# Kernel tuning notes

Hardware: AMD Instinct MI355X
Metric: run time of the kernel (lower is better)

## Reference

```python
import jax, jax.numpy as jnp
import numpy as np

B, T, HID = 1, 1024, 2048
H, DK, DV, M, KW = 16, 128, 128, 128, 4  # heads, key dim, value dim, slots, conv kernel
SCALE = DK ** -0.5
EPS = 1e-5


def short_conv(x, w):
    # causal depthwise conv1d + silu; x: [B,T,C], w: [C,K]
    K = w.shape[1]
    xp = jnp.pad(x, ((0, 0), (K - 1, 0), (0, 0)))
    t = x.shape[1]
    y = sum(xp[:, i:i + t] * w[:, i] for i in range(K))
    return jax.nn.silu(y)


def l2norm(x):
    return x * jax.lax.rsqrt(jnp.sum(x * x, axis=-1, keepdims=True) + 1e-6)


def gsa2_scan(q, k, v, w, g, beta):
    # q,k: [B,T,H,DK]  v: [B,T,H,DV]  w,g: [B,T,H,M]  beta: [B,T,H]
    b = q.shape[0]
    tm = lambda x: jnp.moveaxis(x, 1, 0)  # time-major
    Sk0 = jnp.zeros((b, H, DK, M), q.dtype)  # key->slot memory
    Sv0 = jnp.zeros((b, H, M, DV), q.dtype)  # slot->value memory

    def step(carry, xs):
        Sk, Sv = carry
        q_t, k_t, v_t, w_t, g_t, b_t = xs
        gt = jnp.exp(g_t)  # [B,H,M] gate in (0,1) since g = logsigmoid(.)
        bw = b_t[:, :, None] * w_t  # beta-scaled slot write address [B,H,M]
        Sk = Sk * gt[:, :, None, :] + k_t[..., :, None] * bw[:, :, None, :]
        Sv = Sv * gt[..., None] + bw[..., None] * v_t[:, :, None, :]
        s = jnp.einsum('bhd,bhdm->bhm', q_t, Sk) * SCALE
        a = jax.nn.softmax(s, axis=-1)
        o_t = jnp.einsum('bhm,bhmd->bhd', a, Sv)
        return (Sk, Sv), o_t

    (_, _), o = jax.lax.scan(step, (Sk0, Sv0),
                             (tm(q), tm(k), tm(v), tm(w), tm(g), tm(beta)))
    return jnp.moveaxis(o, 0, 1)  # [B,T,H,DV]


def reference(hidden_states, Wq, Wk, Wv, Ww, cq, ck, cv,
              Wf1, Wf2, Wb, Wg1, Wg2, bg2, norm_w, Wo):
    h = hidden_states  # [B,T,HID]
    q = short_conv(h @ Wq, cq)
    k = short_conv(h @ Wk, ck)
    v = short_conv(h @ Wv, cv)
    w = short_conv(h @ Ww, cv)  # source applies v_conv1d to w (faithful)
    g = jax.nn.log_sigmoid((h @ Wf1) @ Wf2)   # [B,T,H*M]
    beta = jax.nn.sigmoid(h @ Wb)             # [B,T,H]
    rs = lambda x, d: x.reshape(x.shape[0], x.shape[1], -1, d)
    q, k = rs(q, DK), rs(k, DK)
    v = rs(v, DV)
    w = l2norm(rs(w, M))
    g = rs(g, M)
    o = gsa2_scan(q, k, v, w, g, beta)        # [B,T,H,DV]
    gate = rs((h @ Wg1) @ Wg2 + bg2, DV)
    # FusedRMSNormGated with sigmoid activation
    o = o * jax.lax.rsqrt(jnp.mean(o * o, axis=-1, keepdims=True) + EPS)
    o = o * norm_w * jax.nn.sigmoid(gate)
    o = o.reshape(o.shape[0], o.shape[1], -1)
    return o @ Wo


def setup_inputs() -> dict:
    key = jax.random.key(0)
    ks = jax.random.split(key, 16)
    s = 0.02
    return {
        'hidden_states': jax.random.normal(ks[0], (B, T, HID), jnp.float32),
        'Wq': jax.random.normal(ks[1], (HID, H * DK), jnp.float32) * s,
        'Wk': jax.random.normal(ks[2], (HID, H * DK), jnp.float32) * s,
        'Wv': jax.random.normal(ks[3], (HID, H * DV), jnp.float32) * s,
        'Ww': jax.random.normal(ks[4], (HID, H * M), jnp.float32) * s,
        'cq': jax.random.normal(ks[5], (H * DK, KW), jnp.float32) * 0.2,
        'ck': jax.random.normal(ks[6], (H * DK, KW), jnp.float32) * 0.2,
        'cv': jax.random.normal(ks[7], (H * DV, KW), jnp.float32) * 0.2,
        'Wf1': jax.random.normal(ks[8], (HID, DV), jnp.float32) * s,
        'Wf2': jax.random.normal(ks[9], (DV, H * M), jnp.float32) * s,
        'Wb': jax.random.normal(ks[10], (HID, H), jnp.float32) * s,
        'Wg1': jax.random.normal(ks[11], (HID, DV), jnp.float32) * s,
        'Wg2': jax.random.normal(ks[12], (DV, H * DV), jnp.float32) * s,
        'bg2': jnp.zeros((H * DV,), jnp.float32),
        'norm_w': jnp.ones((DV,), jnp.float32),
        'Wo': jax.random.normal(ks[13], (H * DV, HID), jnp.float32) * s,
    }
```

## Files before the change

### kernel.cpp

```cpp
#include <hip/hip_runtime.h>
#include <hip/hip_bf16.h>
#include <stdint.h>

typedef unsigned short u16;
typedef __attribute__((ext_vector_type(8))) short bf16x8;
typedef __attribute__((ext_vector_type(4))) short bf16x4;
typedef __attribute__((ext_vector_type(4))) float f32x4;

#define DEV static __device__ __forceinline__

DEV u16 f2bf(float f){
  union { float f; unsigned u; } x; x.f = f;
  unsigned r = x.u + 0x7fffu + ((x.u >> 16) & 1u);
  return (u16)(r >> 16);
}

DEV float bf2f(u16 u){
  union { unsigned u; float f; } x; x.u = ((unsigned)u) << 16; return x.f;
}

DEV bf16x8 ldfrag(const u16* p){
  bf16x4 a = *(const bf16x4*)p;
  bf16x4 b = *(const bf16x4*)(p+4);
  bf16x8 r;
  r[0]=a[0]; r[1]=a[1]; r[2]=a[2]; r[3]=a[3];
  r[4]=b[0]; r[5]=b[1]; r[6]=b[2]; r[7]=b[3];
  return r;
}

DEV bf16x4 cvt4(float a, float b, float c, float d){
  bf16x4 r; r[0]=(short)f2bf(a); r[1]=(short)f2bf(b); r[2]=(short)f2bf(c); r[3]=(short)f2bf(d);
  return r;
}

DEV void g2l16(const void* g, void* l){
  __builtin_amdgcn_global_load_lds((const __attribute__((address_space(1))) unsigned int*)g,
                                   (__attribute__((address_space(3))) unsigned int*)l,
                                   16, 0, 0);
}

__global__ __launch_bounds__(256)
void transp64_k(const float* __restrict__ Wq, const float* __restrict__ Wk,
                const float* __restrict__ Wv, const float* __restrict__ Ww,
                const float* __restrict__ Wo, u16* __restrict__ WcatT, u16* __restrict__ WoT,
                const float* __restrict__ hX, u16* __restrict__ h_bf,
                const float* __restrict__ Wf1, const float* __restrict__ Wg1,
                const float* __restrict__ Wf2, const float* __restrict__ Wg2,
                const float* __restrict__ Wb,
                u16* __restrict__ WfgT, u16* __restrict__ Wf2T, u16* __restrict__ Wg2T){
  __shared__ float tile[64*65];
  const int z = blockIdx.z;
  if (z == 5){
    int idx = ((blockIdx.y*32 + blockIdx.x)*256 + threadIdx.x)*8;
    float4 v0 = *(const float4*)&hX[idx];
    float4 v1 = *(const float4*)&hX[idx+4];
    ushort4 o0, o1;
    o0.x=f2bf(v0.x); o0.y=f2bf(v0.y); o0.z=f2bf(v0.z); o0.w=f2bf(v0.w);
    o1.x=f2bf(v1.x); o1.y=f2bf(v1.y); o1.z=f2bf(v1.z); o1.w=f2bf(v1.w);
    *(ushort4*)&h_bf[idx]   = o0;
    *(ushort4*)&h_bf[idx+4] = o1;
    return;
  }
  if (z == 10){
    int rem = blockIdx.y*32 + blockIdx.x;
    if (rem >= 256) return;
    int cx = rem & 63, cy = rem >> 6;
    const int x = threadIdx.x & 31, y0 = threadIdx.x >> 5;
    int k = cx*32 + x;
#pragma unroll
    for (int j=0;j<4;j++){
      int rpad = cy*32 + y0 + j*8;
      float v = (rpad < 16) ? Wb[(size_t)k*16 + rpad] : 0.f;
      WfgT[(size_t)(256+rpad)*2048 + k] = f2bf(v);
    }
    return;
  }
  if (z >= 6){
    int rem = blockIdx.y*32 + blockIdx.x;
    if (rem >= 256) return;
    const float* src; u16* dst; int R, C, cx, cy;
    if (z==6){      src=Wf1; dst=WfgT;                  R=2048; C=128;  cx=rem&3;  cy=rem>>2; }
    else if (z==7){ src=Wg1; dst=WfgT+(size_t)128*2048; R=2048; C=128;  cx=rem&3;  cy=rem>>2; }
    else if (z==8){ src=Wf2; dst=Wf2T;                  R=128;  C=2048; cx=rem>>2; cy=rem&3; }
    else {          src=Wg2; dst=Wg2T;                  R=128;  C=2048; cx=rem>>2; cy=rem&3; }
    const int c0 = cx*32, r0 = cy*32;
    const int x = threadIdx.x & 31, y0 = threadIdx.x >> 5;
#pragma unroll
    for (int j=0;j<4;j++){
      int r = y0 + j*8;
      tile[r*33 + x] = src[(size_t)(r0+r)*C + c0 + x];
    }
    __syncthreads();
#pragma unroll
    for (int j=0;j<4;j++){
      int cc = y0 + j*8;
      dst[(size_t)(c0+cc)*R + r0 + x] = f2bf(tile[x*33 + cc]);
    }
    return;
  }
  const float* src = (z==0)?Wq:((z==1)?Wk:((z==2)?Wv:((z==3)?Ww:Wo)));
  u16* dst = (z<4) ? (WcatT + (size_t)z*4194304) : WoT;
  const int c0 = blockIdx.x*64, r0 = blockIdx.y*64;
#pragma unroll
  for (int p=0;p<4;p++){
    int i = threadIdx.x + p*256;
    int r = i>>4, c4 = (i&15)<<2;
    *(float4*)&tile[r*65 + c4] = *(const float4*)&src[(size_t)(r0+r)*2048 + c0 + c4];
  }
  __syncthreads();
#pragma unroll
  for (int p=0;p<4;p++){
    int i = threadIdx.x + p*256;
    int cc = i>>4, r4 = (i&15)<<2;
    ushort4 o;
    o.x = f2bf(tile[(r4+0)*65 + cc]); o.y = f2bf(tile[(r4+1)*65 + cc]);
    o.z = f2bf(tile[(r4+2)*65 + cc]); o.w = f2bf(tile[(r4+3)*65 + cc]);
    *(ushort4*)&dst[(size_t)(c0+cc)*2048 + r0 + r4] = o;
  }
}

template<bool OBF>
__global__ __launch_bounds__(256)
void gemm4_k(const u16* __restrict__ A, const u16* __restrict__ B, void* __restrict__ Cp,
             int K, int lda, int ldb, int ldc){
  __shared__ u16 As[2][128*64];
  __shared__ u16 Bs[2][128*64];
  const int m0 = blockIdx.y*128, n0 = blockIdx.x*128;
  const int tid = threadIdx.x;
  const int wave = tid>>6, lane = tid&63, lr = lane&15, kg = lane>>4;
  const int wm = wave>>1, wn = wave&1;
  const f32x4 vz = {0.f,0.f,0.f,0.f};
  f32x4 acc[4][4];
#pragma unroll
  for (int a=0;a<4;a++)
#pragma unroll
    for (int b=0;b<4;b++) acc[a][b]=vz;

#define STAGE4(buf, k0) do { \
    _Pragma("unroll") \
    for (int p=0;p<4;p++){ \
      int chunk = tid + p*256, r_ = chunk>>3, ci = chunk&7; \
      g2l16(A + (size_t)(m0+r_)*lda + (k0) + ((ci^(r_&7))<<3), &As[buf][chunk*8]); \
    } \
    _Pragma("unroll") \
    for (int p=0;p<4;p++){ \
      int chunk = tid + p*256, r_ = chunk>>3, ci = chunk&7; \
      g2l16(B + (size_t)(n0+r_)*ldb + (k0) + ((ci^(r_&7))<<3), &Bs[buf][chunk*8]); \
    } \
  } while(0)

  const int nt = K>>6;
  STAGE4(0, 0);
  STAGE4(1, 64);
  for (int t=0; t<nt; ++t){
    const int buf = t&1;
    if (t < nt-1) asm volatile("s_waitcnt vmcnt(8)" ::: "memory");
    else          asm volatile("s_waitcnt vmcnt(0)" ::: "memory");
    asm volatile("s_barrier" ::: "memory");
#pragma unroll
    for (int ks=0; ks<2; ++ks){
      bf16x8 af[4], bfv[4];
#pragma unroll
      for (int mi=0;mi<4;mi++){
        int r = wm*64+mi*16+lr;
        af[mi] = *(const bf16x8*)&As[buf][r*64 + (((ks*4+kg)^(r&7))<<3)];
      }
#pragma unroll
      for (int ni=0;ni<4;ni++){
        int r = wn*64+ni*16+lr;
        bfv[ni] = *(const bf16x8*)&Bs[buf][r*64 + (((ks*4+kg)^(r&7))<<3)];
      }
      asm volatile("s_waitcnt lgkmcnt(0)" ::: "memory");
      __builtin_amdgcn_sched_barrier(0);
      __builtin_amdgcn_s_setprio(1);
#pragma unroll
      for (int mi=0;mi<4;mi++)
#pragma unroll
        for (int ni=0;ni<4;ni++)
          acc[mi][ni] = __builtin_amdgcn_mfma_f32_16x16x32_bf16(af[mi], bfv[ni], acc[mi][ni], 0, 0, 0);
      __builtin_amdgcn_s_setprio(0);
      __builtin_amdgcn_sched_barrier(0);
      asm volatile("s_barrier" ::: "memory");
    }
    if (t+2 < nt) STAGE4(buf, (t+2)<<6);
  }
#undef STAGE4
#pragma unroll
  for (int mi=0;mi<4;mi++)
#pragma unroll
    for (int ni=0;ni<4;ni++)
#pragma unroll
      for (int vv=0;vv<4;vv++){
        int row = m0 + wm*64 + mi*16 + kg*4 + vv;
        int col = n0 + wn*64 + ni*16 + lr;
        if (OBF) ((u16*)Cp)[(size_t)row*ldc + col] = f2bf(acc[mi][ni][vv]);
        else     ((float*)Cp)[(size_t)row*ldc + col] = acc[mi][ni][vv];
      }
}

__global__ __launch_bounds__(256)
void gemm4sk_k(const u16* __restrict__ A, const u16* __restrict__ B, float* __restrict__ out,
               int Khalf, int lda, int ldb, int ldc){
  __shared__ u16 As[2][128*64];
  __shared__ u16 Bs[2][128*64];
  const int m0 = blockIdx.y*128, n0 = blockIdx.x*128;
  const int kbase = blockIdx.z*Khalf;
  const int tid = threadIdx.x;
  const int wave = tid>>6, lane = tid&63, lr = lane&15, kg = lane>>4;
  const int wm = wave>>1, wn = wave&1;
  const f32x4 vz = {0.f,0.f,0.f,0.f};
  f32x4 acc[4][4];
#pragma unroll
  for (int a=0;a<4;a++)
#pragma unroll
    for (int b=0;b<4;b++) acc[a][b]=vz;

#define STAGE4(buf, k0) do { \
    _Pragma("unroll") \
    for (int p=0;p<4;p++){ \
      int chunk = tid + p*256, r_ = chunk>>3, ci = chunk&7; \
      g2l16(A + (size_t)(m0+r_)*lda + (k0) + ((ci^(r_&7))<<3), &As[buf][chunk*8]); \
    } \
    _Pragma("unroll") \
    for (int p=0;p<4;p++){ \
      int chunk = tid + p*256, r_ = chunk>>3, ci = chunk&7; \
      g2l16(B + (size_t)(n0+r_)*ldb + (k0) + ((ci^(r_&7))<<3), &Bs[buf][chunk*8]); \
    } \
  } while(0)

  const int nt = Khalf>>6;
  STAGE4(0, kbase);
  STAGE4(1, kbase+64);
  for (int t=0; t<nt; ++t){
    const int buf = t&1;
    if (t < nt-1) asm volatile("s_waitcnt vmcnt(8)" ::: "memory");
    else          asm volatile("s_waitcnt vmcnt(0)" ::: "memory");
    asm volatile("s_barrier" ::: "memory");
#pragma unroll
    for (int ks=0; ks<2; ++ks){
      bf16x8 af[4], bfv[4];
#pragma unroll
      for (int mi=0;mi<4;mi++){
        int r = wm*64+mi*16+lr;
        af[mi] = *(const bf16x8*)&As[buf][r*64 + (((ks*4+kg)^(r&7))<<3)];
      }
#pragma unroll
      for (int ni=0;ni<4;ni++){
        int r = wn*64+ni*16+lr;
        bfv[ni] = *(const bf16x8*)&Bs[buf][r*64 + (((ks*4+kg)^(r&7))<<3)];
// ... 66 lines not shown
  if (zz == 0){
#pragma unroll
    for (int ni=0;ni<4;ni++){
      float p[4][4]; float s[4];
#pragma unroll
      for (int mi=0;mi<4;mi++){
        float run = 0.f;
#pragma unroll
        for (int vv=0;vv<4;vv++){
          float v = acc[mi][ni][vv];
          v = fminf(v,0.f) - __logf(1.f + __expf(-fabsf(v)));
          run += v; p[mi][vv] = run;
        }
        s[mi] = run;
      }
      float M = 0.f; float base[4];
#pragma unroll
      for (int mi=0;mi<4;mi++){
        float a0 = __shfl(s[mi], lr);
        float a1 = __shfl(s[mi], lr+16);
        float a2 = __shfl(s[mi], lr+32);
        float a3 = __shfl(s[mi], lr+48);
        float before = 0.f;
        if (kg>0) before += a0;
        if (kg>1) before += a1;
        if (kg>2) before += a2;
        base[mi] = M + before;
        M += a0+a1+a2+a3;
      }
#pragma unroll
      for (int mi=0;mi<4;mi++)
#pragma unroll
        for (int vv=0;vv<4;vv++){
          int row = m0 + wr*64 + mi*16 + kg*4 + vv;
          int col = n0 + wc*64 + ni*16 + lr;
          Ccg[(size_t)row*2048 + col] = base[mi] + p[mi][vv];
        }
    }
  } else {
#pragma unroll
    for (int mi=0;mi<4;mi++)
#pragma unroll
      for (int ni=0;ni<4;ni++)
#pragma unroll
        for (int vv=0;vv<4;vv++){
          int row = m0 + wr*64 + mi*16 + kg*4 + vv;
          int col = n0 + wc*64 + ni*16 + lr;
          Cgate[(size_t)row*2048 + col] = f2bf(acc[mi][ni][vv]);
        }
  }
}

__global__ __launch_bounds__(256)
void gemmsk_k(const u16* __restrict__ A, const u16* __restrict__ B, u16* __restrict__ P,
              int lda, int ldb){
  __shared__ u16 As[128*32];
  __shared__ u16 Bs[128*32];
  const int m0 = blockIdx.y*128, n0 = blockIdx.x*128;
  const int kbase = blockIdx.z*128;
  const int tid = threadIdx.x;
  const int lane = tid & 63, wave = tid >> 6;
  const int wr = wave >> 1, wc = wave & 1;
  const int lr = lane & 15, kg = lane >> 4;
  const f32x4 vzero = {0.f,0.f,0.f,0.f};
  f32x4 acc[4][4];
#pragma unroll
  for (int a=0;a<4;a++)
#pragma unroll
    for (int b=0;b<4;b++) acc[a][b] = vzero;
  const int r0 = tid>>2, s0 = tid&3;
  for (int k0=kbase;k0<kbase+128;k0+=32){
    __syncthreads();
    g2l16(A + (size_t)(m0+r0)*lda + k0 + s0*8, (u16*)As + (size_t)tid*8);
    g2l16(B + (size_t)(n0+r0)*ldb + k0 + s0*8, (u16*)Bs + (size_t)tid*8);
    g2l16(A + (size_t)(m0+r0+64)*lda + k0 + s0*8, (u16*)As + (size_t)(tid+256)*8);
    g2l16(B + (size_t)(n0+r0+64)*ldb + k0 + s0*8, (u16*)Bs + (size_t)(tid+256)*8);
    __syncthreads();
    bf16x8 af[4], bfv[4];
#pragma unroll
    for (int mi=0;mi<4;mi++) af[mi]  = *(const bf16x8*)(As + (wr*64+mi*16+lr)*32 + kg*8);
#pragma unroll
    for (int ni=0;ni<4;ni++) bfv[ni] = *(const bf16x8*)(Bs + (wc*64+ni*16+lr)*32 + kg*8);
#pragma unroll
    for (int mi=0;mi<4;mi++)
#pragma unroll
      for (int ni=0;ni<4;ni++)
        acc[mi][ni] = __builtin_amdgcn_mfma_f32_16x16x32_bf16(af[mi], bfv[ni], acc[mi][ni], 0, 0, 0);
  }
#pragma unroll
  for (int mi=0;mi<4;mi++)
#pragma unroll
    for (int ni=0;ni<4;ni++)
#pragma unroll
      for (int vv=0;vv<4;vv++){
        int row = m0 + wr*64 + mi*16 + kg*4 + vv;
        int col = n0 + wc*64 + ni*16 + lr;
        P[(size_t)blockIdx.z*393216 + (size_t)row*384 + col] = f2bf(acc[mi][ni][vv]);
      }
}

__global__ __launch_bounds__(256)
void reduceb_k(const u16* __restrict__ P, u16* __restrict__ out, float* __restrict__ betab){
  int i4 = (blockIdx.x*256 + threadIdx.x)*4;
  float s0=0.f, s1=0.f, s2=0.f, s3=0.f;
#pragma unroll
  for (int z=0;z<16;z++){
    ushort4 p = *(const ushort4*)&P[(size_t)z*393216 + i4];
    s0+=bf2f(p.x); s1+=bf2f(p.y); s2+=bf2f(p.z); s3+=bf2f(p.w);
  }
  ushort4 o; o.x=f2bf(s0); o.y=f2bf(s1); o.z=f2bf(s2); o.w=f2bf(s3);
  *(ushort4*)&out[i4] = o;
  int col = i4 % 384;
  if (col >= 256 && col < 272){
    int row = i4 / 384;
    float* bp = &betab[row*16 + (col-256)];
    bp[0] = 1.f/(1.f+__expf(-s0));
    bp[1] = 1.f/(1.f+__expf(-s1));
    bp[2] = 1.f/(1.f+__expf(-s2));
    bp[3] = 1.f/(1.f+__expf(-s3));
  }
}

__global__ __launch_bounds__(256)
void conv_k(const u16* __restrict__ raw, const float* __restrict__ cq,
            const float* __restrict__ ck, const float* __restrict__ cv,
            const float* __restrict__ betab,
            u16* __restrict__ qo, u16* __restrict__ ko,
            u16* __restrict__ vo, u16* __restrict__ bwout){
  __shared__ float red[2][2][4];
  int idx = blockIdx.x*256 + threadIdx.x;
  int cgl = idx & 8191, tb = idx >> 13;
  int which = cgl >> 11, cc = cgl & 2047;
  const float* wt = (which==0)?cq:((which==1)?ck:cv);
  float4 w4 = *(const float4*)&wt[cc*4];
  int t0 = tb*4;
  float x[7];
#pragma unroll
  for (int j=0;j<7;j++){
    int t = t0 - 3 + j;
    x[j] = (t >= 0) ? bf2f(raw[(size_t)t*8192 + cgl]) : 0.f;
  }
  float y[4];
#pragma unroll
  for (int j=0;j<4;j++){
    float yy = x[j]*w4.x + x[j+1]*w4.y + x[j+2]*w4.z + x[j+3]*w4.w;
    y[j] = yy / (1.f + __expf(-yy));
  }
  if (which < 3){
    u16* outb = (which==0)?qo:((which==1)?ko:vo);
#pragma unroll
    for (int j=0;j<4;j++)
      outb[(size_t)(t0+j)*2048 + cc] = f2bf(y[j]);
  } else {
    const int hh = threadIdx.x >> 7;
    const int wh = (threadIdx.x >> 6) & 1;
    float ss[4];
#pragma unroll
    for (int j=0;j<4;j++){
      float s = y[j]*y[j];
#pragma unroll
      for (int off=1;off<64;off<<=1) s += __shfl_xor(s, off);
      ss[j] = s;
    }
    if ((threadIdx.x & 63) == 0){
#pragma unroll
      for (int j=0;j<4;j++) red[hh][wh][j] = ss[j];
    }
    __syncthreads();
    const int h = cc >> 7;
#pragma unroll
    for (int j=0;j<4;j++){
      float tot = red[hh][0][j] + red[hh][1][j];
      float r = rsqrtf(tot + 1e-6f) * betab[(t0+j)*16 + h];
      bwout[(size_t)(t0+j)*2048 + cc] = f2bf(y[j]*r);
    }
  }
}

__global__ __launch_bounds__(256)
void phaseA_k(const u16* __restrict__ k, const u16* __restrict__ v,
              const u16* __restrict__ bw, const float* __restrict__ cg,
              u16* __restrict__ DSkT, u16* __restrict__ DSvT){
  __shared__ u16 UT[128*68];
  __shared__ u16 KT[128*68];
  __shared__ u16 VT[128*68];
  __shared__ float Gt[128];
  const int bx=blockIdx.x, h=bx&15, c=bx>>4, tid=threadIdx.x;
  const int w=tid>>6, lane=tid&63, lr=lane&15, kg=lane>>4;
  if (tid<128) Gt[tid] = cg[(size_t)(c*64+63)*2048 + h*128 + tid];
  __syncthreads();
#pragma unroll
  for (int j=0;j<8;j++){
    int f4=tid+j*256, r=f4>>5, c4=(f4&31)<<2;
    size_t g=(size_t)(c*64+r)*2048 + h*128 + c4;
    ushort4 kv=*(const ushort4*)&k[g];
    ushort4 vv=*(const ushort4*)&v[g];
    ushort4 bv=*(const ushort4*)&bw[g];
    float4 cv=*(const float4*)&cg[g];
    float u0=bf2f(bv.x)*__expf(Gt[c4+0]-cv.x);
    float u1=bf2f(bv.y)*__expf(Gt[c4+1]-cv.y);
    float u2=bf2f(bv.z)*__expf(Gt[c4+2]-cv.z);
    float u3=bf2f(bv.w)*__expf(Gt[c4+3]-cv.w);
    KT[(c4+0)*68+r]=kv.x; KT[(c4+1)*68+r]=kv.y;
    KT[(c4+2)*68+r]=kv.z; KT[(c4+3)*68+r]=kv.w;
    VT[(c4+0)*68+r]=vv.x; VT[(c4+1)*68+r]=vv.y;
    VT[(c4+2)*68+r]=vv.z; VT[(c4+3)*68+r]=vv.w;
    UT[(c4+0)*68+r]=f2bf(u0);   UT[(c4+1)*68+r]=f2bf(u1);
    UT[(c4+2)*68+r]=f2bf(u2);   UT[(c4+3)*68+r]=f2bf(u3);
  }
  __syncthreads();
  const f32x4 vz = {0.f,0.f,0.f,0.f};
  {
    f32x4 acc[2][8];
#pragma unroll
    for (int a=0;a<2;a++)
#pragma unroll
      for (int b=0;b<8;b++) acc[a][b]=vz;
#pragma unroll
    for (int ks=0;ks<2;ks++){
      bf16x8 a0=ldfrag(&UT[(w*32   +lr)*68 + ks*32+kg*8]);
      bf16x8 a1=ldfrag(&UT[(w*32+16+lr)*68 + ks*32+kg*8]);
#pragma unroll
      for (int nj=0;nj<8;nj++){
        bf16x8 b=ldfrag(&KT[(nj*16+lr)*68 + ks*32+kg*8]);
        acc[0][nj]=__builtin_amdgcn_mfma_f32_16x16x32_bf16(a0,b,acc[0][nj],0,0,0);
        acc[1][nj]=__builtin_amdgcn_mfma_f32_16x16x32_bf16(a1,b,acc[1][nj],0,0,0);
      }
    }
#pragma unroll
    for (int mi2=0;mi2<2;mi2++)
#pragma unroll
      for (int nj=0;nj<8;nj++)
#pragma unroll
        for (int vv2=0;vv2<4;vv2++)
          DSkT[(size_t)bx*16384 + (size_t)(w*32+mi2*16+kg*4+vv2)*128 + nj*16+lr] = f2bf(acc[mi2][nj][vv2]);
  }
  {
    f32x4 acc[2][8];
#pragma unroll
    for (int a=0;a<2;a++)
#pragma unroll
      for (int b=0;b<8;b++) acc[a][b]=vz;
#pragma unroll
    for (int ks=0;ks<2;ks++){
      bf16x8 a0=ldfrag(&VT[(w*32   +lr)*68 + ks*32+kg*8]);
      bf16x8 a1=ldfrag(&VT[(w*32+16+lr)*68 + ks*32+kg*8]);
#pragma unroll
      for (int nj=0;nj<8;nj++){
        bf16x8 b=ldfrag(&UT[(nj*16+lr)*68 + ks*32+kg*8]);
        acc[0][nj]=__builtin_amdgcn_mfma_f32_16x16x32_bf16(a0,b,acc[0][nj],0,0,0);
        acc[1][nj]=__builtin_amdgcn_mfma_f32_16x16x32_bf16(a1,b,acc[1][nj],0,0,0);
      }
    }
#pragma unroll
    for (int mi2=0;mi2<2;mi2++)
#pragma unroll
      for (int nj=0;nj<8;nj++)
#pragma unroll
        for (int vv2=0;vv2<4;vv2++)
          DSvT[(size_t)bx*16384 + (size_t)(w*32+mi2*16+kg*4+vv2)*128 + nj*16+lr] = f2bf(acc[mi2][nj][vv2]);
  }
}

__global__ __launch_bounds__(256)
void phaseB_k(const u16* __restrict__ DSk, const u16* __restrict__ DSv,
              const float* __restrict__ cg, u16* __restrict__ Sk0, u16* __restrict__ Sv0){
  unsigned idx = blockIdx.x*256u + threadIdx.x;
  int sel  = idx >> 18;
  int h    = (idx >> 14) & 15;
  int flat = idx & 16383;
  int mdec = sel ? (flat & 127) : (flat >> 7);
  const u16* DS = sel ? DSv : DSk;
  u16* S = sel ? Sv0 : Sk0;
  float cur = 0.f;
  for (int c=0;c<16;c++){
    size_t sb = ((size_t)(c*16+h))*16384 + flat;
    S[sb] = f2bf(cur);
    float gd = __expf(cg[(size_t)(c*64+63)*2048 + h*128 + mdec]);
    cur = cur*gd + bf2f(DS[sb]);
  }
}

__global__ __launch_bounds__(256)
void phaseC_k(const u16* __restrict__ q, const u16* __restrict__ k,
              const u16* __restrict__ v, const u16* __restrict__ bw,
              const float* __restrict__ cg, const u16* __restrict__ SkT,
              const u16* __restrict__ SvT, const u16* __restrict__ gate,
              const float* __restrict__ bg2, const float* __restrict__ nw,
              u16* __restrict__ Obf){
  __shared__ u16 Qb[64*132];
  __shared__ u16 KV[8704];
  __shared__ u16 Bws[64*132];
  __shared__ u16 BwT[128*68];
  __shared__ u16 Ssb[64*68];
  __shared__ u16 SkL[128*132];
  __shared__ u16 SvL[128*132];
  __shared__ float cgm[128];
  __shared__ float ecgm[128];
  const int bx=blockIdx.x, h=bx&15, c=bx>>4, tid=threadIdx.x;
  const int w=tid>>6, lane=tid&63, lr=lane&15, kg=lane>>4;
  const float SCALE = 0.088388347648318447f;
  const f32x4 vz = {0.f,0.f,0.f,0.f};
  if (tid<128){ float t=cg[(size_t)(c*64+31)*2048 + h*128 + tid]; cgm[tid]=t; ecgm[tid]=__expf(t); }
  __syncthreads();
#pragma unroll
  for (int j=0;j<8;j++){
    int f4=tid+j*256, r=f4>>5, c4=(f4&31)<<2;
    size_t g=(size_t)(c*64+r)*2048 + h*128 + c4;
    *(ushort4*)&Qb[r*132+c4] = *(const ushort4*)&q[g];
    *(ushort4*)&KV[r*132+c4] = *(const ushort4*)&k[g];
    ushort4 bv=*(const ushort4*)&bw[g];
    float4 cv=*(const float4*)&cg[g];
    float b0=bf2f(bv.x)*__expf(cgm[c4+0]-cv.x);
    float b1=bf2f(bv.y)*__expf(cgm[c4+1]-cv.y);
    float b2=bf2f(bv.z)*__expf(cgm[c4+2]-cv.z);
    float b3=bf2f(bv.w)*__expf(cgm[c4+3]-cv.w);
    bf16x4 bb = cvt4(b0,b1,b2,b3);
    *(bf16x4*)&Bws[r*132+c4] = bb;
    BwT[(c4+0)*68+r]=(u16)bb[0]; BwT[(c4+1)*68+r]=(u16)bb[1];
    BwT[(c4+2)*68+r]=(u16)bb[2]; BwT[(c4+3)*68+r]=(u16)bb[3];
  }
  __syncthreads();
  {
    f32x4 acc1[4];
#pragma unroll
    for (int a=0;a<4;a++) acc1[a]=vz;
#pragma unroll
    for (int ks=0;ks<4;ks++){
      bf16x8 aq = ldfrag(&Qb[(w*16+lr)*132 + ks*32+kg*8]);
#pragma unroll
      for (int ni=0;ni<4;ni++){
        bf16x8 bk = ldfrag(&KV[(ni*16+lr)*132 + ks*32+kg*8]);
        acc1[ni]=__builtin_amdgcn_mfma_f32_16x16x32_bf16(aq,bk,acc1[ni],0,0,0);
      }
    }
#pragma unroll
    for (int ni=0;ni<4;ni++)
#pragma unroll
      for (int vv2=0;vv2<4;vv2++){
        int row=w*16+kg*4+vv2, col=ni*16+lr;
        Ssb[row*68+col] = (col<=row) ? f2bf(acc1[ni][vv2]) : (u16)0;
      }
  }
  __syncthreads();
#pragma unroll
  for (int j=0;j<8;j++){
    int f4=tid+j*256, r=f4>>5, c4=(f4&31)<<2;
    ushort4 vv=*(const ushort4*)&v[(size_t)(c*64+r)*2048 + h*128 + c4];
    KV[(c4+0)*68+r]=vv.x; KV[(c4+1)*68+r]=vv.y;
    KV[(c4+2)*68+r]=vv.z; KV[(c4+3)*68+r]=vv.w;
  }
#pragma unroll
  for (int j=0;j<16;j++){
    int f4=tid+j*256, r=f4>>5, c4=(f4&31)<<2;
    ushort4 s4=*(const ushort4*)&SkT[(size_t)bx*16384 + (size_t)r*128 + c4];
    float em=ecgm[r];
    *(bf16x4*)&SkL[r*132+c4]=cvt4(bf2f(s4.x)*em, bf2f(s4.y)*em, bf2f(s4.z)*em, bf2f(s4.w)*em);
  }
#pragma unroll
  for (int j=0;j<16;j++){
    int f4=tid+j*256, r=f4>>5, c4=(f4&31)<<2;
    ushort4 s4=*(const ushort4*)&SvT[(size_t)bx*16384 + (size_t)r*128 + c4];
    *(bf16x4*)&SvL[r*132+c4]=cvt4(bf2f(s4.x)*ecgm[c4+0], bf2f(s4.y)*ecgm[c4+1],
                                  bf2f(s4.z)*ecgm[c4+2], bf2f(s4.w)*ecgm[c4+3]);
  }
  f32x4 zac[8];
#pragma unroll
  for (int a=0;a<8;a++) zac[a]=vz;
#pragma unroll
  for (int ks=0;ks<2;ks++){
    bf16x8 as_ = ldfrag(&Ssb[(w*16+lr)*68 + ks*32+kg*8]);
#pragma unroll
    for (int ni=0;ni<8;ni++){
      bf16x8 bb = ldfrag(&BwT[(ni*16+lr)*68 + ks*32+kg*8]);
      zac[ni]=__builtin_amdgcn_mfma_f32_16x16x32_bf16(as_,bb,zac[ni],0,0,0);
    }
  }
  __syncthreads();
#pragma unroll
  for (int dt=0;dt<4;dt++){
    bf16x8 aq = ldfrag(&Qb[(w*16+lr)*132 + dt*32+kg*8]);
#pragma unroll
    for (int ni=0;ni<8;ni++){
      bf16x8 bs = ldfrag(&SkL[(ni*16+lr)*132 + dt*32+kg*8]);
      zac[ni]=__builtin_amdgcn_mfma_f32_16x16x32_bf16(aq,bs,zac[ni],0,0,0);
    }
  }
  float dec[4][8], zz[4][8];
#pragma unroll
  for (int vv2=0;vv2<4;vv2++)
#pragma unroll
    for (int ni=0;ni<8;ni++) zz[vv2][ni]=zac[ni][vv2];
#pragma unroll
  for (int vv2=0;vv2<4;vv2++){
    size_t gr=(size_t)(c*64+w*16+kg*4+vv2)*2048 + h*128;
#pragma unroll
    for (int ni=0;ni<8;ni++){
      float cgv = cg[gr + ni*16+lr];
      dec[vv2][ni] = __expf(cgv - cgm[ni*16+lr]);
    }
  }
#pragma unroll
  for (int vv2=0;vv2<4;vv2++){
// ... 51 lines not shown
  }
#pragma unroll
  for (int mt=0;mt<4;mt++){
    bf16x8 aa = ldfrag(&Qb[(w*16+lr)*132 + mt*32+kg*8]);
#pragma unroll
    for (int ni=0;ni<8;ni++){
      bf16x8 bs = ldfrag(&SvL[(ni*16+lr)*132 + mt*32+kg*8]);
      oac[ni]=__builtin_amdgcn_mfma_f32_16x16x32_bf16(aa,bs,oac[ni],0,0,0);
    }
  }
#pragma unroll
  for (int vv2=0;vv2<4;vv2++){
    float ss = 0.f;
#pragma unroll
    for (int ni=0;ni<8;ni++) ss += oac[ni][vv2]*oac[ni][vv2];
    ss += __shfl_xor(ss,1); ss += __shfl_xor(ss,2);
    ss += __shfl_xor(ss,4); ss += __shfl_xor(ss,8);
    float rr = rsqrtf(ss*(1.f/128.f) + 1e-5f);
    int row = c*64 + w*16 + kg*4 + vv2;
#pragma unroll
    for (int ni=0;ni<8;ni++){
      int colh = ni*16+lr;
      int col  = h*128 + colh;
      float g = bf2f(gate[(size_t)row*2048 + col]) + bg2[col];
      float val = oac[ni][vv2]*rr*nw[colh]*(1.f/(1.f+__expf(-g)));
      Obf[(size_t)row*2048 + col] = f2bf(val);
    }
  }
}

extern "C" void kernel_launch(void* const* d_in, const int* in_sizes, int n_in,
                              void* d_out, int out_size, void* d_ws, size_t ws_size,
                              hipStream_t stream){
  (void)in_sizes; (void)n_in; (void)out_size; (void)ws_size;
  const float* hX   = (const float*)d_in[0];
  const float* Wq   = (const float*)d_in[1];
  const float* Wk   = (const float*)d_in[2];
  const float* Wv   = (const float*)d_in[3];
  const float* Ww   = (const float*)d_in[4];
  const float* cq   = (const float*)d_in[5];
  const float* ck   = (const float*)d_in[6];
  const float* cv   = (const float*)d_in[7];
  const float* Wf1  = (const float*)d_in[8];
  const float* Wf2  = (const float*)d_in[9];
  const float* Wb   = (const float*)d_in[10];
  const float* Wg1  = (const float*)d_in[11];
  const float* Wg2  = (const float*)d_in[12];
  const float* bg2  = (const float*)d_in[13];
  const float* nw   = (const float*)d_in[14];
  const float* Wo   = (const float*)d_in[15];
  char* ws = (char*)d_ws;
  u16*   h_bf  = (u16*)  (ws + 0);
  u16*   WcatT = (u16*)  (ws + 4194304);
  u16*   Sk0   = (u16*)  (ws + 4194304);
  u16*   Sv0   = (u16*)  (ws + 20971520);
  u16*   WoT   = (u16*)  (ws + 37748736);
  u16*   Wf2T  = (u16*)  (ws + 47185920);
  u16*   Wg2T  = (u16*)  (ws + 47710208);
  u16*   qkvw  = (u16*)  (ws + 48234496);
  u16*   DSk   = (u16*)  (ws + 48234496);
  u16*   DSv   = (u16*)  (ws + 56623104);
  u16*   gateb = (u16*)  (ws + 65011712);
  u16*   qb    = (u16*)  (ws + 81788928);
  u16*   kb    = (u16*)  (ws + 90177536);
  u16*   vb    = (u16*)  (ws + 98566144);
  u16*   P8    = (u16*)  (ws + 106954752);
  u16*   bwb   = (u16*)  (ws + 119537664);
  u16*   f1g1  = (u16*)  (ws + 123731968);
  u16*   WfgT  = (u16*)  (ws + 124518400);
  float* cgb   = (float*)(ws + 132644864);
  float* betab = (float*)(ws + 141033472);
  u16*   Obf   = (u16*)  (ws + 141099008);
  float* outp  = (float*)d_out;

  transp64_k<<<dim3(32,32,11),256,0,stream>>>(Wq, Wk, Wv, Ww, Wo, WcatT, WoT, hX, h_bf,
                                              Wf1, Wg1, Wf2, Wg2, Wb, WfgT, Wf2T, Wg2T);

  gemm4_k<true><<<dim3(64,8),256,0,stream>>>(h_bf, WcatT, qkvw, 2048, 2048, 2048, 8192);
  gemmsk_k<<<dim3(3,8,16),256,0,stream>>>(h_bf, WfgT, P8, 2048, 2048);
  reduceb_k<<<384,256,0,stream>>>(P8, f1g1, betab);
  gemmg_k<<<dim3(16,8,2),256,0,stream>>>(f1g1, Wf2T, Wg2T, cgb, gateb);

  conv_k<<<8192,256,0,stream>>>(qkvw, cq, ck, cv, betab, qb, kb, vb, bwb);

  phaseA_k<<<256,256,0,stream>>>(kb, vb, bwb, cgb, DSk, DSv);
  phaseB_k<<<2048,256,0,stream>>>(DSk, DSv, cgb, Sk0, Sv0);
  phaseC_k<<<256,256,0,stream>>>(qb, kb, vb, bwb, cgb, Sk0, Sv0, gateb, bg2, nw, Obf);

  hipMemsetAsync(outp, 0, (size_t)1024*2048*4, stream);
  gemm4sk_k<<<dim3(16,8,2),256,0,stream>>>(Obf, WoT, outp, 1024, 2048, 2048, 2048);
}
```

Measured before the change: 176.4 us.

## Fuse short conv and l2norm into chunk phase A and phase C kernels

```diff
diff --git a/kernel.cpp b/kernel.cpp
--- a/kernel.cpp
+++ b/kernel.cpp
@@ -37,6 +37,31 @@
   __builtin_amdgcn_global_load_lds((const __attribute__((address_space(1))) unsigned int*)g,
                                    (__attribute__((address_space(3))) unsigned int*)l,
                                    16, 0, 0);
+}
+
+DEV void conv4si(const u16* __restrict__ raw, const float* __restrict__ wt,
+                 int t, int chg, float* y){
+  const int cc = chg & 2047;
+  float4 w0 = *(const float4*)&wt[(cc+0)*4];
+  float4 w1 = *(const float4*)&wt[(cc+1)*4];
+  float4 w2 = *(const float4*)&wt[(cc+2)*4];
+  float4 w3 = *(const float4*)&wt[(cc+3)*4];
+  float wa0[4]={w0.x,w0.y,w0.z,w0.w}, wa1[4]={w1.x,w1.y,w1.z,w1.w};
+  float wa2[4]={w2.x,w2.y,w2.z,w2.w}, wa3[4]={w3.x,w3.y,w3.z,w3.w};
+  float a0=0.f,a1=0.f,a2=0.f,a3=0.f;
+#pragma unroll
+  for (int jj=0;jj<4;jj++){
+    int tt = t-3+jj;
+    if (tt >= 0){
+      ushort4 x = *(const ushort4*)&raw[(size_t)tt*8192 + chg];
+      a0 += bf2f(x.x)*wa0[jj];
+      a1 += bf2f(x.y)*wa1[jj];
+      a2 += bf2f(x.z)*wa2[jj];
+      a3 += bf2f(x.w)*wa3[jj];
+    }
+  }
+  y[0]=a0/(1.f+__expf(-a0)); y[1]=a1/(1.f+__expf(-a1));
+  y[2]=a2/(1.f+__expf(-a2)); y[3]=a3/(1.f+__expf(-a3));
 }
 
 __global__ __launch_bounds__(256)
@@ -437,64 +462,9 @@
 }
 
 __global__ __launch_bounds__(256)
-void conv_k(const u16* __restrict__ raw, const float* __restrict__ cq,
-            const float* __restrict__ ck, const float* __restrict__ cv,
-            const float* __restrict__ betab,
-            u16* __restrict__ qo, u16* __restrict__ ko,
-            u16* __restrict__ vo, u16* __restrict__ bwout){
-  __shared__ float red[2][2][4];
-  int idx = blockIdx.x*256 + threadIdx.x;
-  int cgl = idx & 8191, tb = idx >> 13;
-  int which = cgl >> 11, cc = cgl & 2047;
-  const float* wt = (which==0)?cq:((which==1)?ck:cv);
-  float4 w4 = *(const float4*)&wt[cc*4];
-  int t0 = tb*4;
-  float x[7];
-#pragma unroll
-  for (int j=0;j<7;j++){
-    int t = t0 - 3 + j;
-    x[j] = (t >= 0) ? bf2f(raw[(size_t)t*8192 + cgl]) : 0.f;
-  }
-  float y[4];
-#pragma unroll
-  for (int j=0;j<4;j++){
-    float yy = x[j]*w4.x + x[j+1]*w4.y + x[j+2]*w4.z + x[j+3]*w4.w;
-    y[j] = yy / (1.f + __expf(-yy));
-  }
-  if (which < 3){
-    u16* outb = (which==0)?qo:((which==1)?ko:vo);
-#pragma unroll
-    for (int j=0;j<4;j++)
-      outb[(size_t)(t0+j)*2048 + cc] = f2bf(y[j]);
-  } else {
-    const int hh = threadIdx.x >> 7;
-    const int wh = (threadIdx.x >> 6) & 1;
-    float ss[4];
-#pragma unroll
-    for (int j=0;j<4;j++){
-      float s = y[j]*y[j];
-#pragma unroll
-      for (int off=1;off<64;off<<=1) s += __shfl_xor(s, off);
-      ss[j] = s;
-    }
-    if ((threadIdx.x & 63) == 0){
-#pragma unroll
-      for (int j=0;j<4;j++) red[hh][wh][j] = ss[j];
-    }
-    __syncthreads();
-    const int h = cc >> 7;
-#pragma unroll
-    for (int j=0;j<4;j++){
-      float tot = red[hh][0][j] + red[hh][1][j];
-      float r = rsqrtf(tot + 1e-6f) * betab[(t0+j)*16 + h];
-      bwout[(size_t)(t0+j)*2048 + cc] = f2bf(y[j]*r);
-    }
-  }
-}
-
-__global__ __launch_bounds__(256)
-void phaseA_k(const u16* __restrict__ k, const u16* __restrict__ v,
-              const u16* __restrict__ bw, const float* __restrict__ cg,
+void phaseA_k(const u16* __restrict__ raw, const float* __restrict__ ck,
+              const float* __restrict__ cv, const float* __restrict__ betab,
+              const float* __restrict__ cg,
               u16* __restrict__ DSkT, u16* __restrict__ DSvT){
   __shared__ u16 UT[128*68];
   __shared__ u16 KT[128*68];
@@ -507,21 +477,26 @@
 #pragma unroll
   for (int j=0;j<8;j++){
     int f4=tid+j*256, r=f4>>5, c4=(f4&31)<<2;
-    size_t g=(size_t)(c*64+r)*2048 + h*128 + c4;
-    ushort4 kv=*(const ushort4*)&k[g];
-    ushort4 vv=*(const ushort4*)&v[g];
-    ushort4 bv=*(const ushort4*)&bw[g];
-    float4 cv=*(const float4*)&cg[g];
-    float u0=bf2f(bv.x)*__expf(Gt[c4+0]-cv.x);
-    float u1=bf2f(bv.y)*__expf(Gt[c4+1]-cv.y);
-    float u2=bf2f(bv.z)*__expf(Gt[c4+2]-cv.z);
-    float u3=bf2f(bv.w)*__expf(Gt[c4+3]-cv.w);
-    KT[(c4+0)*68+r]=kv.x; KT[(c4+1)*68+r]=kv.y;
-    KT[(c4+2)*68+r]=kv.z; KT[(c4+3)*68+r]=kv.w;
-    VT[(c4+0)*68+r]=vv.x; VT[(c4+1)*68+r]=vv.y;
-    VT[(c4+2)*68+r]=vv.z; VT[(c4+3)*68+r]=vv.w;
-    UT[(c4+0)*68+r]=f2bf(u0);   UT[(c4+1)*68+r]=f2bf(u1);
-    UT[(c4+2)*68+r]=f2bf(u2);   UT[(c4+3)*68+r]=f2bf(u3);
+    int t = c*64+r, ch = h*128+c4;
+    float yk[4], yv[4], yw[4];
+    conv4si(raw, ck, t, 2048+ch, yk);
+    conv4si(raw, cv, t, 4096+ch, yv);
+    conv4si(raw, cv, t, 6144+ch, yw);
+    float ss = yw[0]*yw[0]+yw[1]*yw[1]+yw[2]*yw[2]+yw[3]*yw[3];
+    ss += __shfl_xor(ss,1); ss += __shfl_xor(ss,2); ss += __shfl_xor(ss,4);
+    ss += __shfl_xor(ss,8); ss += __shfl_xor(ss,16);
+    float rr = rsqrtf(ss + 1e-6f) * betab[t*16+h];
+    float4 cgv = *(const float4*)&cg[(size_t)t*2048 + ch];
+    float u0 = yw[0]*rr*__expf(Gt[c4+0]-cgv.x);
+    float u1 = yw[1]*rr*__expf(Gt[c4+1]-cgv.y);
+    float u2 = yw[2]*rr*__expf(Gt[c4+2]-cgv.z);
+    float u3 = yw[3]*rr*__expf(Gt[c4+3]-cgv.w);
+    KT[(c4+0)*68+r]=f2bf(yk[0]); KT[(c4+1)*68+r]=f2bf(yk[1]);
+    KT[(c4+2)*68+r]=f2bf(yk[2]); KT[(c4+3)*68+r]=f2bf(yk[3]);
+    VT[(c4+0)*68+r]=f2bf(yv[0]); VT[(c4+1)*68+r]=f2bf(yv[1]);
+    VT[(c4+2)*68+r]=f2bf(yv[2]); VT[(c4+3)*68+r]=f2bf(yv[3]);
+    UT[(c4+0)*68+r]=f2bf(u0);    UT[(c4+1)*68+r]=f2bf(u1);
+    UT[(c4+2)*68+r]=f2bf(u2);    UT[(c4+3)*68+r]=f2bf(u3);
   }
   __syncthreads();
   const f32x4 vz = {0.f,0.f,0.f,0.f};
@@ -597,8 +572,9 @@
 }
 
 __global__ __launch_bounds__(256)
-void phaseC_k(const u16* __restrict__ q, const u16* __restrict__ k,
-              const u16* __restrict__ v, const u16* __restrict__ bw,
+void phaseC_k(const u16* __restrict__ raw, const float* __restrict__ cq,
+              const float* __restrict__ ck, const float* __restrict__ cv,
+              const float* __restrict__ betab,
               const float* __restrict__ cg, const u16* __restrict__ SkT,
               const u16* __restrict__ SvT, const u16* __restrict__ gate,
               const float* __restrict__ bg2, const float* __restrict__ nw,
@@ -621,15 +597,22 @@
 #pragma unroll
   for (int j=0;j<8;j++){
     int f4=tid+j*256, r=f4>>5, c4=(f4&31)<<2;
-    size_t g=(size_t)(c*64+r)*2048 + h*128 + c4;
-    *(ushort4*)&Qb[r*132+c4] = *(const ushort4*)&q[g];
-    *(ushort4*)&KV[r*132+c4] = *(const ushort4*)&k[g];
-    ushort4 bv=*(const ushort4*)&bw[g];
-    float4 cv=*(const float4*)&cg[g];
-    float b0=bf2f(bv.x)*__expf(cgm[c4+0]-cv.x);
-    float b1=bf2f(bv.y)*__expf(cgm[c4+1]-cv.y);
-    float b2=bf2f(bv.z)*__expf(cgm[c4+2]-cv.z);
-    float b3=bf2f(bv.w)*__expf(cgm[c4+3]-cv.w);
+    int t = c*64+r, ch = h*128+c4;
+    float yq[4], yk[4], yw[4];
+    conv4si(raw, cq, t, ch,      yq);
+    conv4si(raw, ck, t, 2048+ch, yk);
+    conv4si(raw, cv, t, 6144+ch, yw);
+    float ss = yw[0]*yw[0]+yw[1]*yw[1]+yw[2]*yw[2]+yw[3]*yw[3];
+    ss += __shfl_xor(ss,1); ss += __shfl_xor(ss,2); ss += __shfl_xor(ss,4);
+    ss += __shfl_xor(ss,8); ss += __shfl_xor(ss,16);
+    float rr = rsqrtf(ss + 1e-6f) * betab[t*16+h];
+    *(bf16x4*)&Qb[r*132+c4] = cvt4(yq[0],yq[1],yq[2],yq[3]);
+    *(bf16x4*)&KV[r*132+c4] = cvt4(yk[0],yk[1],yk[2],yk[3]);
+    float4 cgv = *(const float4*)&cg[(size_t)t*2048 + ch];
+    float b0 = yw[0]*rr*__expf(cgm[c4+0]-cgv.x);
+    float b1 = yw[1]*rr*__expf(cgm[c4+1]-cgv.y);
+    float b2 = yw[2]*rr*__expf(cgm[c4+2]-cgv.z);
+    float b3 = yw[3]*rr*__expf(cgm[c4+3]-cgv.w);
     bf16x4 bb = cvt4(b0,b1,b2,b3);
     *(bf16x4*)&Bws[r*132+c4] = bb;
     BwT[(c4+0)*68+r]=(u16)bb[0]; BwT[(c4+1)*68+r]=(u16)bb[1];
@@ -661,9 +644,11 @@
 #pragma unroll
   for (int j=0;j<8;j++){
     int f4=tid+j*256, r=f4>>5, c4=(f4&31)<<2;
-    ushort4 vv=*(const ushort4*)&v[(size_t)(c*64+r)*2048 + h*128 + c4];
-    KV[(c4+0)*68+r]=vv.x; KV[(c4+1)*68+r]=vv.y;
-    KV[(c4+2)*68+r]=vv.z; KV[(c4+3)*68+r]=vv.w;
+    int t = c*64+r, ch = h*128+c4;
+    float yv[4];
+    conv4si(raw, cv, t, 4096+ch, yv);
+    KV[(c4+0)*68+r]=f2bf(yv[0]); KV[(c4+1)*68+r]=f2bf(yv[1]);
+    KV[(c4+2)*68+r]=f2bf(yv[2]); KV[(c4+3)*68+r]=f2bf(yv[3]);
   }
 #pragma unroll
   for (int j=0;j<16;j++){
@@ -827,14 +812,10 @@
   u16*   Wf2T  = (u16*)  (ws + 47185920);
   u16*   Wg2T  = (u16*)  (ws + 47710208);
   u16*   qkvw  = (u16*)  (ws + 48234496);
-  u16*   DSk   = (u16*)  (ws + 48234496);
-  u16*   DSv   = (u16*)  (ws + 56623104);
   u16*   gateb = (u16*)  (ws + 65011712);
-  u16*   qb    = (u16*)  (ws + 81788928);
-  u16*   kb    = (u16*)  (ws + 90177536);
-  u16*   vb    = (u16*)  (ws + 98566144);
+  u16*   DSk   = (u16*)  (ws + 81788928);
+  u16*   DSv   = (u16*)  (ws + 90177536);
   u16*   P8    = (u16*)  (ws + 106954752);
-  u16*   bwb   = (u16*)  (ws + 119537664);
   u16*   f1g1  = (u16*)  (ws + 123731968);
   u16*   WfgT  = (u16*)  (ws + 124518400);
   float* cgb   = (float*)(ws + 132644864);
@@ -850,11 +831,9 @@
   reduceb_k<<<384,256,0,stream>>>(P8, f1g1, betab);
   gemmg_k<<<dim3(16,8,2),256,0,stream>>>(f1g1, Wf2T, Wg2T, cgb, gateb);
 
-  conv_k<<<8192,256,0,stream>>>(qkvw, cq, ck, cv, betab, qb, kb, vb, bwb);
-
-  phaseA_k<<<256,256,0,stream>>>(kb, vb, bwb, cgb, DSk, DSv);
+  phaseA_k<<<256,256,0,stream>>>(qkvw, ck, cv, betab, cgb, DSk, DSv);
   phaseB_k<<<2048,256,0,stream>>>(DSk, DSv, cgb, Sk0, Sv0);
-  phaseC_k<<<256,256,0,stream>>>(qb, kb, vb, bwb, cgb, Sk0, Sv0, gateb, bg2, nw, Obf);
+  phaseC_k<<<256,256,0,stream>>>(qkvw, cq, ck, cv, betab, cgb, Sk0, Sv0, gateb, bg2, nw, Obf);
 
   hipMemsetAsync(outp, 0, (size_t)1024*2048*4, stream);
   gemm4sk_k<<<dim3(16,8,2),256,0,stream>>>(Obf, WoT, outp, 1024, 2048, 2048, 2048);
```

Measured after the change: 232.5 us. 31.8% more time.

## Fold f1/g1/beta projection into main QKVW GEMM and vectorize conv kernel

Applied to the files above, without the earlier changes.

```diff
diff --git a/kernel.cpp b/kernel.cpp
--- a/kernel.cpp
+++ b/kernel.cpp
@@ -119,10 +119,10 @@
   }
 }
 
-template<bool OBF>
 __global__ __launch_bounds__(256)
-void gemm4_k(const u16* __restrict__ A, const u16* __restrict__ B, void* __restrict__ Cp,
-             int K, int lda, int ldb, int ldc){
+void gemmQ_k(const u16* __restrict__ A, const u16* __restrict__ B, u16* __restrict__ C,
+             u16* __restrict__ f1g1o, float* __restrict__ betab,
+             int K, int lda, int ldb){
   __shared__ u16 As[2][128*64];
   __shared__ u16 Bs[2][128*64];
   const int m0 = blockIdx.y*128, n0 = blockIdx.x*128;
@@ -193,8 +193,15 @@
       for (int vv=0;vv<4;vv++){
         int row = m0 + wm*64 + mi*16 + kg*4 + vv;
         int col = n0 + wn*64 + ni*16 + lr;
-        if (OBF) ((u16*)Cp)[(size_t)row*ldc + col] = f2bf(acc[mi][ni][vv]);
-        else     ((float*)Cp)[(size_t)row*ldc + col] = acc[mi][ni][vv];
+        float val = acc[mi][ni][vv];
+        if (col < 8192){
+          C[(size_t)row*8192 + col] = f2bf(val);
+        } else {
+          int c8 = col - 8192;
+          f1g1o[(size_t)row*384 + c8] = f2bf(val);
+          if (c8 >= 256 && c8 < 272)
+            betab[row*16 + (c8-256)] = 1.f/(1.f+__expf(-val));
+        }
       }
 }
 
@@ -367,127 +374,68 @@
 }
 
 __global__ __launch_bounds__(256)
-void gemmsk_k(const u16* __restrict__ A, const u16* __restrict__ B, u16* __restrict__ P,
-              int lda, int ldb){
-  __shared__ u16 As[128*32];
-  __shared__ u16 Bs[128*32];
-  const int m0 = blockIdx.y*128, n0 = blockIdx.x*128;
-  const int kbase = blockIdx.z*128;
-  const int tid = threadIdx.x;
-  const int lane = tid & 63, wave = tid >> 6;
-  const int wr = wave >> 1, wc = wave & 1;
-  const int lr = lane & 15, kg = lane >> 4;
-  const f32x4 vzero = {0.f,0.f,0.f,0.f};
-  f32x4 acc[4][4];
-#pragma unroll
-  for (int a=0;a<4;a++)
-#pragma unroll
-    for (int b=0;b<4;b++) acc[a][b] = vzero;
-  const int r0 = tid>>2, s0 = tid&3;
-  for (int k0=kbase;k0<kbase+128;k0+=32){
-    __syncthreads();
-    g2l16(A + (size_t)(m0+r0)*lda + k0 + s0*8, (u16*)As + (size_t)tid*8);
-    g2l16(B + (size_t)(n0+r0)*ldb + k0 + s0*8, (u16*)Bs + (size_t)tid*8);
-    g2l16(A + (size_t)(m0+r0+64)*lda + k0 + s0*8, (u16*)As + (size_t)(tid+256)*8);
-    g2l16(B + (size_t)(n0+r0+64)*ldb + k0 + s0*8, (u16*)Bs + (size_t)(tid+256)*8);
-    __syncthreads();
-    bf16x8 af[4], bfv[4];
-#pragma unroll
-    for (int mi=0;mi<4;mi++) af[mi]  = *(const bf16x8*)(As + (wr*64+mi*16+lr)*32 + kg*8);
-#pragma unroll
-    for (int ni=0;ni<4;ni++) bfv[ni] = *(const bf16x8*)(Bs + (wc*64+ni*16+lr)*32 + kg*8);
-#pragma unroll
-    for (int mi=0;mi<4;mi++)
-#pragma unroll
-      for (int ni=0;ni<4;ni++)
-        acc[mi][ni] = __builtin_amdgcn_mfma_f32_16x16x32_bf16(af[mi], bfv[ni], acc[mi][ni], 0, 0, 0);
-  }
-#pragma unroll
-  for (int mi=0;mi<4;mi++)
-#pragma unroll
-    for (int ni=0;ni<4;ni++)
-#pragma unroll
-      for (int vv=0;vv<4;vv++){
-        int row = m0 + wr*64 + mi*16 + kg*4 + vv;
-        int col = n0 + wc*64 + ni*16 + lr;
-        P[(size_t)blockIdx.z*393216 + (size_t)row*384 + col] = f2bf(acc[mi][ni][vv]);
-      }
-}
-
-__global__ __launch_bounds__(256)
-void reduceb_k(const u16* __restrict__ P, u16* __restrict__ out, float* __restrict__ betab){
-  int i4 = (blockIdx.x*256 + threadIdx.x)*4;
-  float s0=0.f, s1=0.f, s2=0.f, s3=0.f;
-#pragma unroll
-  for (int z=0;z<16;z++){
-    ushort4 p = *(const ushort4*)&P[(size_t)z*393216 + i4];
-    s0+=bf2f(p.x); s1+=bf2f(p.y); s2+=bf2f(p.z); s3+=bf2f(p.w);
-  }
-  ushort4 o; o.x=f2bf(s0); o.y=f2bf(s1); o.z=f2bf(s2); o.w=f2bf(s3);
-  *(ushort4*)&out[i4] = o;
-  int col = i4 % 384;
-  if (col >= 256 && col < 272){
-    int row = i4 / 384;
-    float* bp = &betab[row*16 + (col-256)];
-    bp[0] = 1.f/(1.f+__expf(-s0));
-    bp[1] = 1.f/(1.f+__expf(-s1));
-    bp[2] = 1.f/(1.f+__expf(-s2));
-    bp[3] = 1.f/(1.f+__expf(-s3));
-  }
-}
-
-__global__ __launch_bounds__(256)
 void conv_k(const u16* __restrict__ raw, const float* __restrict__ cq,
             const float* __restrict__ ck, const float* __restrict__ cv,
             const float* __restrict__ betab,
             u16* __restrict__ qo, u16* __restrict__ ko,
             u16* __restrict__ vo, u16* __restrict__ bwout){
-  __shared__ float red[2][2][4];
   int idx = blockIdx.x*256 + threadIdx.x;
-  int cgl = idx & 8191, tb = idx >> 13;
-  int which = cgl >> 11, cc = cgl & 2047;
+  int g8 = idx & 1023;
+  int tb = idx >> 10;
+  int chg = g8*8;
+  int which = chg >> 11, cc = chg & 2047;
   const float* wt = (which==0)?cq:((which==1)?ck:cv);
-  float4 w4 = *(const float4*)&wt[cc*4];
+  float w[8][4];
+#pragma unroll
+  for (int e=0;e<8;e++){
+    float4 w4 = *(const float4*)&wt[(cc+e)*4];
+    w[e][0]=w4.x; w[e][1]=w4.y; w[e][2]=w4.z; w[e][3]=w4.w;
+  }
   int t0 = tb*4;
-  float x[7];
+  float x[7][8];
 #pragma unroll
   for (int j=0;j<7;j++){
     int t = t0 - 3 + j;
-    x[j] = (t >= 0) ? bf2f(raw[(size_t)t*8192 + cgl]) : 0.f;
-  }
-  float y[4];
-#pragma unroll
-  for (int j=0;j<4;j++){
-    float yy = x[j]*w4.x + x[j+1]*w4.y + x[j+2]*w4.z + x[j+3]*w4.w;
-    y[j] = yy / (1.f + __expf(-yy));
-  }
+    if (t >= 0){
+      bf16x8 xv = *(const bf16x8*)&raw[(size_t)t*8192 + chg];
+#pragma unroll
+      for (int e=0;e<8;e++) x[j][e] = bf2f((u16)xv[e]);
+    } else {
+#pragma unroll
+      for (int e=0;e<8;e++) x[j][e] = 0.f;
+    }
+  }
+  float y[4][8];
+#pragma unroll
+  for (int j=0;j<4;j++)
+#pragma unroll
+    for (int e=0;e<8;e++){
+      float a = x[j][e]*w[e][0] + x[j+1][e]*w[e][1] + x[j+2][e]*w[e][2] + x[j+3][e]*w[e][3];
+      y[j][e] = a/(1.f+__expf(-a));
+    }
   if (which < 3){
     u16* outb = (which==0)?qo:((which==1)?ko:vo);
 #pragma unroll
-    for (int j=0;j<4;j++)
-      outb[(size_t)(t0+j)*2048 + cc] = f2bf(y[j]);
+    for (int j=0;j<4;j++){
+      bf16x8 o;
+#pragma unroll
+      for (int e=0;e<8;e++) o[e] = (short)f2bf(y[j][e]);
+      *(bf16x8*)&outb[(size_t)(t0+j)*2048 + cc] = o;
+    }
   } else {
-    const int hh = threadIdx.x >> 7;
-    const int wh = (threadIdx.x >> 6) & 1;
-    float ss[4];
+    const int h = cc >> 7;
 #pragma unroll
     for (int j=0;j<4;j++){
-      float s = y[j]*y[j];
-#pragma unroll
-      for (int off=1;off<64;off<<=1) s += __shfl_xor(s, off);
-      ss[j] = s;
-    }
-    if ((threadIdx.x & 63) == 0){
-#pragma unroll
-      for (int j=0;j<4;j++) red[hh][wh][j] = ss[j];
-    }
-    __syncthreads();
-    const int h = cc >> 7;
-#pragma unroll
-    for (int j=0;j<4;j++){
-      float tot = red[hh][0][j] + red[hh][1][j];
-      float r = rsqrtf(tot + 1e-6f) * betab[(t0+j)*16 + h];
-      bwout[(size_t)(t0+j)*2048 + cc] = f2bf(y[j]*r);
+      float s = 0.f;
+#pragma unroll
+      for (int e=0;e<8;e++) s += y[j][e]*y[j][e];
+      s += __shfl_xor(s,1); s += __shfl_xor(s,2);
+      s += __shfl_xor(s,4); s += __shfl_xor(s,8);
+      float r = rsqrtf(s + 1e-6f) * betab[(t0+j)*16 + h];
+      bf16x8 o;
+#pragma unroll
+      for (int e=0;e<8;e++) o[e] = (short)f2bf(y[j][e]*r);
+      *(bf16x8*)&bwout[(size_t)(t0+j)*2048 + cc] = o;
     }
   }
 }
@@ -821,36 +769,33 @@
   char* ws = (char*)d_ws;
   u16*   h_bf  = (u16*)  (ws + 0);
   u16*   WcatT = (u16*)  (ws + 4194304);
-  u16*   Sk0   = (u16*)  (ws + 4194304);
-  u16*   Sv0   = (u16*)  (ws + 20971520);
-  u16*   WoT   = (u16*)  (ws + 37748736);
-  u16*   Wf2T  = (u16*)  (ws + 47185920);
-  u16*   Wg2T  = (u16*)  (ws + 47710208);
-  u16*   qkvw  = (u16*)  (ws + 48234496);
-  u16*   DSk   = (u16*)  (ws + 48234496);
-  u16*   DSv   = (u16*)  (ws + 56623104);
-  u16*   gateb = (u16*)  (ws + 65011712);
-  u16*   qb    = (u16*)  (ws + 81788928);
-  u16*   kb    = (u16*)  (ws + 90177536);
-  u16*   vb    = (u16*)  (ws + 98566144);
-  u16*   P8    = (u16*)  (ws + 106954752);
-  u16*   bwb   = (u16*)  (ws + 119537664);
-  u16*   f1g1  = (u16*)  (ws + 123731968);
-  u16*   WfgT  = (u16*)  (ws + 124518400);
-  float* cgb   = (float*)(ws + 132644864);
-  float* betab = (float*)(ws + 141033472);
-  u16*   Obf   = (u16*)  (ws + 141099008);
+  u16*   WfgT  = (u16*)  (ws + 37748736);
+  u16*   WoT   = (u16*)  (ws + 39321600);
+  u16*   Wf2T  = (u16*)  (ws + 47710208);
+  u16*   Wg2T  = (u16*)  (ws + 48234496);
+  u16*   qkvw  = (u16*)  (ws + 48758784);
+  u16*   DSk   = (u16*)  (ws + 48758784);
+  u16*   DSv   = (u16*)  (ws + 57147392);
+  u16*   gateb = (u16*)  (ws + 65536000);
+  u16*   qb    = (u16*)  (ws + 69730304);
+  u16*   kb    = (u16*)  (ws + 73924608);
+  u16*   vb    = (u16*)  (ws + 78118912);
+  u16*   bwb   = (u16*)  (ws + 82313216);
+  u16*   f1g1  = (u16*)  (ws + 86507520);
+  float* cgb   = (float*)(ws + 87293952);
+  float* betab = (float*)(ws + 95682560);
+  u16*   Obf   = (u16*)  (ws + 95748096);
+  u16*   Sk0   = (u16*)  (ws + 99942400);
+  u16*   Sv0   = (u16*)  (ws + 108331008);
   float* outp  = (float*)d_out;
 
   transp64_k<<<dim3(32,32,11),256,0,stream>>>(Wq, Wk, Wv, Ww, Wo, WcatT, WoT, hX, h_bf,
                                               Wf1, Wg1, Wf2, Wg2, Wb, WfgT, Wf2T, Wg2T);
 
-  gemm4_k<true><<<dim3(64,8),256,0,stream>>>(h_bf, WcatT, qkvw, 2048, 2048, 2048, 8192);
-  gemmsk_k<<<dim3(3,8,16),256,0,stream>>>(h_bf, WfgT, P8, 2048, 2048);
-  reduceb_k<<<384,256,0,stream>>>(P8, f1g1, betab);
+  gemmQ_k<<<dim3(67,8),256,0,stream>>>(h_bf, WcatT, qkvw, f1g1, betab, 2048, 2048, 2048);
   gemmg_k<<<dim3(16,8,2),256,0,stream>>>(f1g1, Wf2T, Wg2T, cgb, gateb);
 
-  conv_k<<<8192,256,0,stream>>>(qkvw, cq, ck, cv, betab, qb, kb, vb, bwb);
+  conv_k<<<1024,256,0,stream>>>(qkvw, cq, ck, cv, betab, qb, kb, vb, bwb);
 
   phaseA_k<<<256,256,0,stream>>>(kb, vb, bwb, cgb, DSk, DSv);
   phaseB_k<<<2048,256,0,stream>>>(DSk, DSv, cgb, Sk0, Sv0);
```

New measurement: 198.8 us. 12.7% more time.
